# Optimization experiments

Hardware: AMD Instinct MI355X
Metric: run time of the kernel (lower is better)

Reference implementation:

```python
import jax, jax.numpy as jnp
import numpy as np

EMBED_DIM = 1024
NUM_HEADS = 16
HEAD_DIM = EMBED_DIM // NUM_HEADS


def setup_inputs() -> dict:
    key = jax.random.key(0)
    ks = jax.random.split(key, 9)
    B, T, D = 4, 2048, EMBED_DIM
    s = 1.0 / np.sqrt(D)
    inp = {
        "x": jax.random.normal(ks[0], (B, T, D), dtype=jnp.float32),
        "Wq": jax.random.normal(ks[1], (D, D), dtype=jnp.float32) * s,
        "bq": jnp.zeros((D,), dtype=jnp.float32),
        "Wk": jax.random.normal(ks[2], (D, D), dtype=jnp.float32) * s,
        "bk": jnp.zeros((D,), dtype=jnp.float32),
        "Wv": jax.random.normal(ks[3], (D, D), dtype=jnp.float32) * s,
        "bv": jnp.zeros((D,), dtype=jnp.float32),
        "Wo": jax.random.normal(ks[4], (D, D), dtype=jnp.float32) * s,
        "bo": jnp.zeros((D,), dtype=jnp.float32),
    }
    return inp


def _attn(x, Wq, bq, Wk, bk, Wv, bv, Wo, bo):
    B, T, D = x.shape
    H, Hd = NUM_HEADS, HEAD_DIM
    # projections: Linear uses y = x @ W^T + b; here W stored as (D, D) acting as W^T already
    q = (x @ Wq + bq).reshape(B, T, H, Hd).transpose(0, 2, 1, 3)  # [B,H,T,Hd]
    k = (x @ Wk + bk).reshape(B, T, H, Hd).transpose(0, 2, 1, 3)
    v = (x @ Wv + bv).reshape(B, T, H, Hd).transpose(0, 2, 1, 3)
    scores = jnp.einsum("bhqd,bhkd->bhqk", q, k) / np.sqrt(Hd)  # [B,H,T,T]
    causal = jnp.tril(jnp.ones((T, T), dtype=bool))
    scores = jnp.where(causal, scores, -jnp.inf)
    w = jax.nn.softmax(scores, axis=-1)
    out = jnp.einsum("bhqk,bhkd->bhqd", w, v)  # [B,H,T,Hd]
    out = out.transpose(0, 2, 1, 3).reshape(B, T, D)
    return out @ Wo + bo


def reference(x, Wq, bq, Wk, bk, Wv, bv, Wo, bo):
    return _attn(x, Wq, bq, Wk, bk, Wv, bv, Wo, bo)
```

## Files before the change

### kernel.cpp

```cpp
#include <hip/hip_runtime.h>
#include <cstdint>
#include <cstddef>

#define DI __device__ __forceinline__

typedef unsigned short u16;
typedef short bf16x8 __attribute__((ext_vector_type(8)));
typedef unsigned short u16x8 __attribute__((ext_vector_type(8)));
typedef float f32x4 __attribute__((ext_vector_type(4)));

static constexpr int DMODEL = 1024, T = 2048, BB = 4, NH = 16, HD = 64;
static constexpr int M = BB * T;

static constexpr size_t XB_OFF = 0;
static constexpr size_t WT_OFF = (size_t)M * DMODEL;
static constexpr size_t Q_OFF  = WT_OFF + 4ull * DMODEL * DMODEL;
static constexpr size_t K_OFF  = Q_OFF + (size_t)M * DMODEL;
static constexpr size_t V_OFF  = K_OFF + (size_t)M * DMODEL;
static constexpr size_t O_OFF  = XB_OFF;

DI u16 f2bf(float x) {
  unsigned int u = __builtin_bit_cast(unsigned int, x);
  u += 0x7fffu + ((u >> 16) & 1u);
  return (u16)(u >> 16);
}

DI unsigned int cvtpk_bf16(float a, float b) {
  unsigned int r;
  asm("v_cvt_pk_bf16_f32 %0, %1, %2" : "=v"(r) : "v"(a), "v"(b));
  return r;
}

DI void gld_lds16(const void* g, void* l) {
  __builtin_amdgcn_global_load_lds(
      (const __attribute__((address_space(1))) void*)g,
      (__attribute__((address_space(3))) void*)l, 16, 0, 0);
}

__global__ void k_cast(const float* __restrict__ in, u16* __restrict__ out) {
  size_t i = (size_t)(blockIdx.x * 256 + threadIdx.x) * 8;
  float4 a = *(const float4*)(in + i);
  float4 b = *(const float4*)(in + i + 4);
  u16x8 v;
  v[0] = f2bf(a.x); v[1] = f2bf(a.y); v[2] = f2bf(a.z); v[3] = f2bf(a.w);
  v[4] = f2bf(b.x); v[5] = f2bf(b.y); v[6] = f2bf(b.z); v[7] = f2bf(b.w);
  *(u16x8*)(out + i) = v;
}

__global__ void k_transw(const float* __restrict__ Wq, const float* __restrict__ Wk,
                         const float* __restrict__ Wv, const float* __restrict__ Wo,
                         u16* __restrict__ WtBase) {
  __shared__ u16 tile[32][33];
  const int z = blockIdx.z;
  const float* W = z == 0 ? Wq : (z == 1 ? Wk : (z == 2 ? Wv : Wo));
  u16* Wt = WtBase + (size_t)z * DMODEL * DMODEL;
  int tx = threadIdx.x, ty = threadIdx.y;
  int c = blockIdx.x * 32 + tx;
#pragma unroll
  for (int i = 0; i < 4; ++i) {
    int r = blockIdx.y * 32 + ty + i * 8;
    tile[ty + i * 8][tx] = f2bf(W[(size_t)r * DMODEL + c]);
  }
  __syncthreads();
#pragma unroll
  for (int i = 0; i < 4; ++i) {
    int rw = blockIdx.x * 32 + ty + i * 8;
    Wt[(size_t)rw * DMODEL + blockIdx.y * 32 + tx] = tile[tx][ty + i * 8];
  }
}

template <bool SWAP>
DI void gemm_loop(const u16* __restrict__ A, const u16* __restrict__ Bt,
                  u16* As, u16* Bs, f32x4 (&acc)[4][4], int brow, int bcol, int tid) {
  const int wave = tid >> 6, lane = tid & 63;
  const int g = lane >> 4, l15 = lane & 15;
  const int wr = wave >> 1, wc = wave & 1;
  const int srow = tid >> 3, schunk = tid & 7;

  for (int k0 = 0; k0 < DMODEL; k0 += 64) {
    __syncthreads();
#pragma unroll
    for (int j = 0; j < 4; ++j) {
      int r = j * 32 + srow;
      int cs = (schunk ^ (r & 7)) * 8;
      gld_lds16(A + (size_t)(brow + r) * DMODEL + k0 + cs, (char*)As + j * 4096 + wave * 1024);
      gld_lds16(Bt + (size_t)(bcol + r) * DMODEL + k0 + cs, (char*)Bs + j * 4096 + wave * 1024);
    }
    __syncthreads();
#pragma unroll
    for (int kh = 0; kh < 2; ++kh) {
      bf16x8 af[4], bfr[4];
#pragma unroll
      for (int m = 0; m < 4; ++m) {
        int r = wr * 64 + m * 16 + l15;
        int ch = (kh * 4 + g) ^ (r & 7);
        af[m] = *(const bf16x8*)((const char*)As + r * 128 + ch * 16);
      }
#pragma unroll
      for (int n = 0; n < 4; ++n) {
        int r = wc * 64 + n * 16 + l15;
        int ch = (kh * 4 + g) ^ (r & 7);
        bfr[n] = *(const bf16x8*)((const char*)Bs + r * 128 + ch * 16);
      }
#pragma unroll
      for (int m = 0; m < 4; ++m)
#pragma unroll
        for (int n = 0; n < 4; ++n) {
          if (SWAP)
            acc[m][n] = __builtin_amdgcn_mfma_f32_16x16x32_bf16(bfr[n], af[m], acc[m][n], 0, 0, 0);
          else
            acc[m][n] = __builtin_amdgcn_mfma_f32_16x16x32_bf16(af[m], bfr[n], acc[m][n], 0, 0, 0);
        }
    }
  }
}

__launch_bounds__(256, 2)
__global__ void k_gemm_qkv(const u16* __restrict__ A, const u16* __restrict__ Wt,
                           const float* __restrict__ bq, const float* __restrict__ bk,
                           const float* __restrict__ bv,
                           u16* __restrict__ Qo, u16* __restrict__ Ko,
                           u16* __restrict__ VTo) {
  __shared__ u16 As[128 * 64];
  __shared__ u16 Bs[128 * 64];
  const int z = blockIdx.z;
  const u16* Bt = Wt + (size_t)z * DMODEL * DMODEL;

  const int tid = threadIdx.x;
  const int wave = tid >> 6, lane = tid & 63;
  const int g = lane >> 4, l15 = lane & 15;
  const int brow = blockIdx.x * 128, bcol = blockIdx.y * 128;
  const int wr = wave >> 1, wc = wave & 1;

  f32x4 acc[4][4] = {};

  if (z == 2) {
    gemm_loop<true>(A, Bt, As, Bs, acc, brow, bcol, tid);
#pragma unroll
    for (int m = 0; m < 4; ++m) {
      int trow = brow + wr * 64 + m * 16 + l15;
      int b = trow >> 11, t = trow & 2047;
      int kt = t >> 6, tin = t & 63;
#pragma unroll
      for (int n = 0; n < 4; ++n)
#pragma unroll
        for (int r = 0; r < 4; ++r) {
          int dg = bcol + wc * 64 + n * 16 + g * 4 + r;
          float v = acc[m][n][r] + bv[dg];
          int h = dg >> 6, dd = dg & 63;
          VTo[(((size_t)(b * NH + h) * 32 + kt) << 12) + dd * 64 + tin] = f2bf(v);
        }
    }
  } else {
    gemm_loop<false>(A, Bt, As, Bs, acc, brow, bcol, tid);
    const float* bias = z == 0 ? bq : bk;
    u16* out = z == 0 ? Qo : Ko;
    const float scale = z == 0 ? 0.125f * 1.4426950408889634f : 1.0f;
#pragma unroll
    for (int m = 0; m < 4; ++m)
#pragma unroll
      for (int n = 0; n < 4; ++n) {
        int col = bcol + wc * 64 + n * 16 + l15;
        float bias_v = bias[col];
        int h = col >> 6, d = col & 63;
#pragma unroll
        for (int r = 0; r < 4; ++r) {
          int row = brow + wr * 64 + m * 16 + g * 4 + r;
          int b = row >> 11, t = row & 2047;
          float v = (acc[m][n][r] + bias_v) * scale;
          out[(((size_t)(b * NH + h) * T + t) << 6) + d] = f2bf(v);
        }
      }
  }
}

__launch_bounds__(256, 2)
__global__ void k_gemm_out(const u16* __restrict__ A, const u16* __restrict__ Bt,
                           const float* __restrict__ bias, float* __restrict__ out) {
  __shared__ u16 As[128 * 64];
  __shared__ u16 Bs[128 * 64];
  const int tid = threadIdx.x;
  const int wave = tid >> 6, lane = tid & 63;
  const int g = lane >> 4, l15 = lane & 15;
  const int brow = blockIdx.x * 128, bcol = blockIdx.y * 128;
  const int wr = wave >> 1, wc = wave & 1;

  f32x4 acc[4][4] = {};
  gemm_loop<false>(A, Bt, As, Bs, acc, brow, bcol, tid);

#pragma unroll
  for (int m = 0; m < 4; ++m)
#pragma unroll
    for (int n = 0; n < 4; ++n) {
      int col = bcol + wc * 64 + n * 16 + l15;
      float bias_v = bias[col];
#pragma unroll
      for (int r = 0; r < 4; ++r) {
        int row = brow + wr * 64 + m * 16 + g * 4 + r;
        out[(size_t)row * DMODEL + col] = acc[m][n][r] + bias_v;
      }
    }
}

__launch_bounds__(256, 4)
__global__ void k_attn(const u16* __restrict__ Qw, const u16* __restrict__ Kw,
                       const u16* __restrict__ VTw, u16* __restrict__ Ow) {
  __shared__ u16 Ks[2][64 * 64];
  __shared__ u16 Vt[2][64 * 64];
  __shared__ u16 Ot[64 * 64];

  const int tid = threadIdx.x;
  const int wave = tid >> 6, lane = tid & 63;
  const int g = lane >> 4, l15 = lane & 15;
  const int tl = (l15 & 3) | ((l15 & 4) << 1) | ((l15 & 8) >> 1);
  const int l = blockIdx.x;
  const int xcd = l & 7, w = l >> 3;
  const int bh = xcd + ((w & 7) << 3);
  const int qp = w >> 3;
  const u16* Qb = Qw + (size_t)bh * T * HD;
  const u16* Kb = Kw + (size_t)bh * T * HD;
  const u16* Vb = VTw + (size_t)bh * HD * T;
  const int b = bh >> 4, h = bh & 15;
  const int krow = tid >> 3, kchunk = tid & 7;

  for (int half = 0; half < 2; ++half) {
    const int qt = half == 0 ? (31 - qp) : qp;
    const int ntiles = qt + 1;

    bf16x8 qf[2];
    {
      int qrow = qt * 64 + wave * 16 + l15;
#pragma unroll
      for (int kh = 0; kh < 2; ++kh)
        qf[kh] = *(const bf16x8*)(Qb + (size_t)qrow * HD + kh * 32 + g * 8);
    }

    f32x4 oacc[4] = {};
    float lrun = 0.f;

#pragma unroll
    for (int j = 0; j < 2; ++j) {
      int r = j * 32 + krow;
      gld_lds16(Kb + (size_t)r * HD + (kchunk ^ (r & 7)) * 8,
                (char*)(Ks[0]) + j * 4096 + wave * 1024);
      gld_lds16(Vb + r * 64 + (kchunk ^ (r & 7)) * 8,
                (char*)(Vt[0]) + j * 4096 + wave * 1024);
    }

    for (int kt = 0; kt < ntiles; ++kt) {
      __syncthreads();
      const int cur = kt & 1;
      const bool havenext = (kt + 1 < ntiles);

      if (havenext) {
#pragma unroll
        for (int j = 0; j < 2; ++j) {
          int r = j * 32 + krow;
          gld_lds16(Kb + (size_t)((kt + 1) * 64 + r) * HD + (kchunk ^ (r & 7)) * 8,
                    (char*)(Ks[cur ^ 1]) + j * 4096 + wave * 1024);
          gld_lds16(Vb + ((size_t)(kt + 1) << 12) + r * 64 + (kchunk ^ (r & 7)) * 8,
                    (char*)(Vt[cur ^ 1]) + j * 4096 + wave * 1024);
        }
      }

      bf16x8 kf[2][4];
#pragma unroll
      for (int kh = 0; kh < 2; ++kh)
#pragma unroll
        for (int n = 0; n < 4; ++n) {
          int rr = n * 16 + tl;
          int ch = (kh * 4 + g) ^ (rr & 7);
          kf[kh][n] = *(const bf16x8*)((const char*)(Ks[cur]) + rr * 128 + ch * 16);
        }

      f32x4 s[4] = {};
      __builtin_amdgcn_s_setprio(1);
#pragma unroll
      for (int kh = 0; kh < 2; ++kh)
#pragma unroll
        for (int n = 0; n < 4; ++n)
          s[n] = __builtin_amdgcn_mfma_f32_16x16x32_bf16(kf[kh][n], qf[kh], s[n], 0, 0, 0);
      __builtin_amdgcn_s_setprio(0);

      if (kt == qt) {
        int q_in = wave * 16 + l15;
#pragma unroll
        for (int n = 0; n < 4; ++n)
#pragma unroll
          for (int r = 0; r < 4; ++r) {
            int kv_in = n * 16 + (g & 1) * 8 + (g >> 1) * 4 + r;
            if (kv_in > q_in) s[n][r] = -1e30f;
          }
      }

      float ps0 = 0.f, ps1 = 0.f, ps2 = 0.f, ps3 = 0.f;
#pragma unroll
      for (int n = 0; n < 4; ++n) {
        float p0 = exp2f(s[n][0]);
        float p1 = exp2f(s[n][1]);
        float p2 = exp2f(s[n][2]);
        float p3 = exp2f(s[n][3]);
        s[n][0] = p0; s[n][1] = p1; s[n][2] = p2; s[n][3] = p3;
        ps0 += p0; ps1 += p1; ps2 += p2; ps3 += p3;
      }
      lrun += (ps0 + ps1) + (ps2 + ps3);

      __builtin_amdgcn_s_setprio(1);
#pragma unroll
      for (int kvh = 0; kvh < 2; ++kvh) {
        const int nlo = kvh * 2, nhi = kvh * 2 + 1;
        unsigned int L0 = cvtpk_bf16(s[nlo][0], s[nlo][1]);
        unsigned int L1 = cvtpk_bf16(s[nlo][2], s[nlo][3]);
        unsigned int H0 = cvtpk_bf16(s[nhi][0], s[nhi][1]);
        unsigned int H1 = cvtpk_bf16(s[nhi][2], s[nhi][3]);
        asm volatile("v_permlane32_swap_b32 %0, %1" : "+v"(L0), "+v"(H0));
        asm volatile("v_permlane32_swap_b32 %0, %1" : "+v"(L1), "+v"(H1));
        bf16x8 pb;
        unsigned int* pw = (unsigned int*)&pb;
        pw[0] = L0; pw[1] = L1; pw[2] = H0; pw[3] = H1;

        const int ch = ((kvh * 4 + g) ^ (l15 & 7)) * 16;
#pragma unroll
        for (int n = 0; n < 4; ++n) {
          bf16x8 an = *(const bf16x8*)((const char*)(Vt[cur]) + (n * 16 + l15) * 128 + ch);
          oacc[n] = __builtin_amdgcn_mfma_f32_16x16x32_bf16(an, pb, oacc[n], 0, 0, 0);
        }
      }
      __builtin_amdgcn_s_setprio(0);
    }

    {
      float ltot = lrun;
      ltot += __shfl_xor(ltot, 16);
      ltot += __shfl_xor(ltot, 32);
      float inv = 1.f / ltot;
      char* otb = (char*)Ot;
#pragma unroll
      for (int n = 0; n < 4; ++n)
#pragma unroll
        for (int i = 0; i < 2; ++i) {
          unsigned int w2 = cvtpk_bf16(oacc[n][2 * i] * inv, oacc[n][2 * i + 1] * inv);
          int didx = n * 8 + g * 2 + i;
          int off = (wave * 16 + l15) * 128 + ((didx * 4) ^ ((l15 & 7) << 4));
          *(unsigned int*)(otb + off) = w2;
        }
      __syncthreads();
      int q = tid >> 2, seg = tid & 3;
      uint4 c0 = *(const uint4*)(otb + q * 128 + (((seg * 2) ^ (q & 7)) << 4));
      uint4 c1 = *(const uint4*)(otb + q * 128 + (((seg * 2 + 1) ^ (q & 7)) << 4));
      u16* dst = Ow + ((size_t)b * T + qt * 64 + q) * DMODEL + h * 64 + seg * 16;
      *(uint4*)dst = c0;
      *(uint4*)(dst + 8) = c1;
    }
  }
}

extern "C" void kernel_launch(void* const* d_in, const int* in_sizes, int n_in,
                              void* d_out, int out_size, void* d_ws, size_t ws_size,
                              hipStream_t stream) {
  const float* x  = (const float*)d_in[0];
  const float* Wq = (const float*)d_in[1];
  const float* bq = (const float*)d_in[2];
  const float* Wk = (const float*)d_in[3];
  const float* bk = (const float*)d_in[4];
  const float* Wv = (const float*)d_in[5];
  const float* bv = (const float*)d_in[6];
  const float* Wo = (const float*)d_in[7];
  const float* bo = (const float*)d_in[8];
  float* out = (float*)d_out;
  u16* ws = (u16*)d_ws;

  k_cast<<<4096, 256, 0, stream>>>(x, ws + XB_OFF);
  k_transw<<<dim3(32, 32, 4), dim3(32, 8), 0, stream>>>(Wq, Wk, Wv, Wo, ws + WT_OFF);
  k_gemm_qkv<<<dim3(64, 8, 3), 256, 0, stream>>>(ws + XB_OFF, ws + WT_OFF, bq, bk, bv,
                                                 ws + Q_OFF, ws + K_OFF, ws + V_OFF);
  k_attn<<<1024, 256, 0, stream>>>(ws + Q_OFF, ws + K_OFF, ws + V_OFF, ws + O_OFF);
  k_gemm_out<<<dim3(64, 8), 256, 0, stream>>>(ws + O_OFF, ws + WT_OFF + 3ull * DMODEL * DMODEL,
                                              bo, out);
}
```

Before: 155.1 us.

## Use two waves per attention block, each processing 32 query rows

```diff
diff --git a/kernel.cpp b/kernel.cpp
--- a/kernel.cpp
+++ b/kernel.cpp
@@ -202,7 +202,7 @@
     }
 }
 
-__launch_bounds__(256, 4)
+__launch_bounds__(128, 2)
 __global__ void k_attn(const u16* __restrict__ Qw, const u16* __restrict__ Kw,
                        const u16* __restrict__ VTw, u16* __restrict__ Ow) {
   __shared__ u16 Ks[2][64 * 64];
@@ -221,30 +221,31 @@
   const u16* Kb = Kw + (size_t)bh * T * HD;
   const u16* Vb = VTw + (size_t)bh * HD * T;
   const int b = bh >> 4, h = bh & 15;
-  const int krow = tid >> 3, kchunk = tid & 7;
+  const int srow8 = lane >> 3, schunk = lane & 7;
 
   for (int half = 0; half < 2; ++half) {
     const int qt = half == 0 ? (31 - qp) : qp;
     const int ntiles = qt + 1;
 
-    bf16x8 qf[2];
-    {
-      int qrow = qt * 64 + wave * 16 + l15;
+    bf16x8 qf[2][2];
+#pragma unroll
+    for (int set = 0; set < 2; ++set) {
+      int qrow = qt * 64 + wave * 32 + set * 16 + l15;
 #pragma unroll
       for (int kh = 0; kh < 2; ++kh)
-        qf[kh] = *(const bf16x8*)(Qb + (size_t)qrow * HD + kh * 32 + g * 8);
-    }
-
-    f32x4 oacc[4] = {};
-    float lrun = 0.f;
-
-#pragma unroll
-    for (int j = 0; j < 2; ++j) {
-      int r = j * 32 + krow;
-      gld_lds16(Kb + (size_t)r * HD + (kchunk ^ (r & 7)) * 8,
-                (char*)(Ks[0]) + j * 4096 + wave * 1024);
-      gld_lds16(Vb + r * 64 + (kchunk ^ (r & 7)) * 8,
-                (char*)(Vt[0]) + j * 4096 + wave * 1024);
+        qf[set][kh] = *(const bf16x8*)(Qb + (size_t)qrow * HD + kh * 32 + g * 8);
+    }
+
+    f32x4 oacc[2][4] = {};
+    float lrun0 = 0.f, lrun1 = 0.f;
+
+#pragma unroll
+    for (int j = 0; j < 4; ++j) {
+      int r = j * 16 + wave * 8 + srow8;
+      gld_lds16(Kb + (size_t)r * HD + (schunk ^ (r & 7)) * 8,
+                (char*)(Ks[0]) + j * 2048 + wave * 1024);
+      gld_lds16(Vb + r * 64 + (schunk ^ (r & 7)) * 8,
+                (char*)(Vt[0]) + j * 2048 + wave * 1024);
     }
 
     for (int kt = 0; kt < ntiles; ++kt) {
@@ -254,12 +255,12 @@
 
       if (havenext) {
 #pragma unroll
-        for (int j = 0; j < 2; ++j) {
-          int r = j * 32 + krow;
-          gld_lds16(Kb + (size_t)((kt + 1) * 64 + r) * HD + (kchunk ^ (r & 7)) * 8,
-                    (char*)(Ks[cur ^ 1]) + j * 4096 + wave * 1024);
-          gld_lds16(Vb + ((size_t)(kt + 1) << 12) + r * 64 + (kchunk ^ (r & 7)) * 8,
-                    (char*)(Vt[cur ^ 1]) + j * 4096 + wave * 1024);
+        for (int j = 0; j < 4; ++j) {
+          int r = j * 16 + wave * 8 + srow8;
+          gld_lds16(Kb + (size_t)((kt + 1) * 64 + r) * HD + (schunk ^ (r & 7)) * 8,
+                    (char*)(Ks[cur ^ 1]) + j * 2048 + wave * 1024);
+          gld_lds16(Vb + ((size_t)(kt + 1) << 12) + r * 64 + (schunk ^ (r & 7)) * 8,
+                    (char*)(Vt[cur ^ 1]) + j * 2048 + wave * 1024);
         }
       }
 
@@ -273,84 +274,127 @@
           kf[kh][n] = *(const bf16x8*)((const char*)(Ks[cur]) + rr * 128 + ch * 16);
         }
 
-      f32x4 s[4] = {};
+      f32x4 s[2][4] = {};
       __builtin_amdgcn_s_setprio(1);
 #pragma unroll
       for (int kh = 0; kh < 2; ++kh)
 #pragma unroll
-        for (int n = 0; n < 4; ++n)
-          s[n] = __builtin_amdgcn_mfma_f32_16x16x32_bf16(kf[kh][n], qf[kh], s[n], 0, 0, 0);
+        for (int n = 0; n < 4; ++n) {
+          s[0][n] = __builtin_amdgcn_mfma_f32_16x16x32_bf16(kf[kh][n], qf[0][kh], s[0][n], 0, 0, 0);
+          s[1][n] = __builtin_amdgcn_mfma_f32_16x16x32_bf16(kf[kh][n], qf[1][kh], s[1][n], 0, 0, 0);
+        }
       __builtin_amdgcn_s_setprio(0);
 
       if (kt == qt) {
-        int q_in = wave * 16 + l15;
-#pragma unroll
-        for (int n = 0; n < 4; ++n)
-#pragma unroll
-          for (int r = 0; r < 4; ++r) {
-            int kv_in = n * 16 + (g & 1) * 8 + (g >> 1) * 4 + r;
-            if (kv_in > q_in) s[n][r] = -1e30f;
-          }
-      }
-
-      float ps0 = 0.f, ps1 = 0.f, ps2 = 0.f, ps3 = 0.f;
-#pragma unroll
-      for (int n = 0; n < 4; ++n) {
-        float p0 = exp2f(s[n][0]);
-        float p1 = exp2f(s[n][1]);
-        float p2 = exp2f(s[n][2]);
-        float p3 = exp2f(s[n][3]);
-        s[n][0] = p0; s[n][1] = p1; s[n][2] = p2; s[n][3] = p3;
-        ps0 += p0; ps1 += p1; ps2 += p2; ps3 += p3;
-      }
-      lrun += (ps0 + ps1) + (ps2 + ps3);
+#pragma unroll
+        for (int set = 0; set < 2; ++set) {
+          int q_in = wave * 32 + set * 16 + l15;
+#pragma unroll
+          for (int n = 0; n < 4; ++n)
+#pragma unroll
+            for (int r = 0; r < 4; ++r) {
+              int kv_in = n * 16 + (g & 1) * 8 + (g >> 1) * 4 + r;
+              if (kv_in > q_in) s[set][n][r] = -1e30f;
+            }
+        }
+      }
+
+      {
+        float ps0 = 0.f, ps1 = 0.f, ps2 = 0.f, ps3 = 0.f;
+#pragma unroll
+        for (int n = 0; n < 4; ++n) {
+          float p0 = exp2f(s[0][n][0]);
+          float p1 = exp2f(s[0][n][1]);
+          float p2 = exp2f(s[0][n][2]);
+          float p3 = exp2f(s[0][n][3]);
+          s[0][n][0] = p0; s[0][n][1] = p1; s[0][n][2] = p2; s[0][n][3] = p3;
+          ps0 += p0; ps1 += p1; ps2 += p2; ps3 += p3;
+        }
+        lrun0 += (ps0 + ps1) + (ps2 + ps3);
+      }
+      {
+        float ps0 = 0.f, ps1 = 0.f, ps2 = 0.f, ps3 = 0.f;
+#pragma unroll
+        for (int n = 0; n < 4; ++n) {
+          float p0 = exp2f(s[1][n][0]);
+          float p1 = exp2f(s[1][n][1]);
+          float p2 = exp2f(s[1][n][2]);
+          float p3 = exp2f(s[1][n][3]);
+          s[1][n][0] = p0; s[1][n][1] = p1; s[1][n][2] = p2; s[1][n][3] = p3;
+          ps0 += p0; ps1 += p1; ps2 += p2; ps3 += p3;
+        }
+        lrun1 += (ps0 + ps1) + (ps2 + ps3);
+      }
 
       __builtin_amdgcn_s_setprio(1);
 #pragma unroll
       for (int kvh = 0; kvh < 2; ++kvh) {
         const int nlo = kvh * 2, nhi = kvh * 2 + 1;
-        unsigned int L0 = cvtpk_bf16(s[nlo][0], s[nlo][1]);
-        unsigned int L1 = cvtpk_bf16(s[nlo][2], s[nlo][3]);
-        unsigned int H0 = cvtpk_bf16(s[nhi][0], s[nhi][1]);
-        unsigned int H1 = cvtpk_bf16(s[nhi][2], s[nhi][3]);
-        asm volatile("v_permlane32_swap_b32 %0, %1" : "+v"(L0), "+v"(H0));
-        asm volatile("v_permlane32_swap_b32 %0, %1" : "+v"(L1), "+v"(H1));
-        bf16x8 pb;
-        unsigned int* pw = (unsigned int*)&pb;
-        pw[0] = L0; pw[1] = L1; pw[2] = H0; pw[3] = H1;
+        unsigned int A0 = cvtpk_bf16(s[0][nlo][0], s[0][nlo][1]);
+        unsigned int A1 = cvtpk_bf16(s[0][nlo][2], s[0][nlo][3]);
+        unsigned int B0 = cvtpk_bf16(s[0][nhi][0], s[0][nhi][1]);
+        unsigned int B1 = cvtpk_bf16(s[0][nhi][2], s[0][nhi][3]);
+        asm volatile("v_permlane32_swap_b32 %0, %1" : "+v"(A0), "+v"(B0));
+        asm volatile("v_permlane32_swap_b32 %0, %1" : "+v"(A1), "+v"(B1));
+        bf16x8 pb0;
+        {
+          unsigned int* pw = (unsigned int*)&pb0;
+          pw[0] = A0; pw[1] = A1; pw[2] = B0; pw[3] = B1;
+        }
+        unsigned int C0 = cvtpk_bf16(s[1][nlo][0], s[1][nlo][1]);
+        unsigned int C1 = cvtpk_bf16(s[1][nlo][2], s[1][nlo][3]);
+        unsigned int D0 = cvtpk_bf16(s[1][nhi][0], s[1][nhi][1]);
+        unsigned int D1 = cvtpk_bf16(s[1][nhi][2], s[1][nhi][3]);
+        asm volatile("v_permlane32_swap_b32 %0, %1" : "+v"(C0), "+v"(D0));
+        asm volatile("v_permlane32_swap_b32 %0, %1" : "+v"(C1), "+v"(D1));
+        bf16x8 pb1;
+        {
+          unsigned int* pw = (unsigned int*)&pb1;
+          pw[0] = C0; pw[1] = C1; pw[2] = D0; pw[3] = D1;
+        }
 
         const int ch = ((kvh * 4 + g) ^ (l15 & 7)) * 16;
 #pragma unroll
         for (int n = 0; n < 4; ++n) {
           bf16x8 an = *(const bf16x8*)((const char*)(Vt[cur]) + (n * 16 + l15) * 128 + ch);
-          oacc[n] = __builtin_amdgcn_mfma_f32_16x16x32_bf16(an, pb, oacc[n], 0, 0, 0);
+          oacc[0][n] = __builtin_amdgcn_mfma_f32_16x16x32_bf16(an, pb0, oacc[0][n], 0, 0, 0);
+          oacc[1][n] = __builtin_amdgcn_mfma_f32_16x16x32_bf16(an, pb1, oacc[1][n], 0, 0, 0);
         }
       }
       __builtin_amdgcn_s_setprio(0);
     }
 
     {
-      float ltot = lrun;
-      ltot += __shfl_xor(ltot, 16);
-      ltot += __shfl_xor(ltot, 32);
-      float inv = 1.f / ltot;
+      float lt0 = lrun0;
+      lt0 += __shfl_xor(lt0, 16);
+      lt0 += __shfl_xor(lt0, 32);
+      float lt1 = lrun1;
+      lt1 += __shfl_xor(lt1, 16);
+      lt1 += __shfl_xor(lt1, 32);
+      float inv0 = 1.f / lt0, inv1 = 1.f / lt1;
       char* otb = (char*)Ot;
 #pragma unroll
       for (int n = 0; n < 4; ++n)
 #pragma unroll
         for (int i = 0; i < 2; ++i) {
-          unsigned int w2 = cvtpk_bf16(oacc[n][2 * i] * inv, oacc[n][2 * i + 1] * inv);
           int didx = n * 8 + g * 2 + i;
-          int off = (wave * 16 + l15) * 128 + ((didx * 4) ^ ((l15 & 7) << 4));
-          *(unsigned int*)(otb + off) = w2;
+          int cswz = (didx * 4) ^ ((l15 & 7) << 4);
+          unsigned int w0 = cvtpk_bf16(oacc[0][n][2 * i] * inv0, oacc[0][n][2 * i + 1] * inv0);
+          *(unsigned int*)(otb + (wave * 32 + l15) * 128 + cswz) = w0;
+          unsigned int w1 = cvtpk_bf16(oacc[1][n][2 * i] * inv1, oacc[1][n][2 * i + 1] * inv1);
+          *(unsigned int*)(otb + (wave * 32 + 16 + l15) * 128 + cswz) = w1;
         }
       __syncthreads();
-      int q = tid >> 2, seg = tid & 3;
-      uint4 c0 = *(const uint4*)(otb + q * 128 + (((seg * 2) ^ (q & 7)) << 4));
-      uint4 c1 = *(const uint4*)(otb + q * 128 + (((seg * 2 + 1) ^ (q & 7)) << 4));
-      u16* dst = Ow + ((size_t)b * T + qt * 64 + q) * DMODEL + h * 64 + seg * 16;
-      *(uint4*)dst = c0;
-      *(uint4*)(dst + 8) = c1;
+#pragma unroll
+      for (int i = 0; i < 2; ++i) {
+        int q = i * 32 + (tid >> 2), seg = tid & 3;
+        uint4 c0 = *(const uint4*)(otb + q * 128 + (((seg * 2) ^ (q & 7)) << 4));
+        uint4 c1 = *(const uint4*)(otb + q * 128 + (((seg * 2 + 1) ^ (q & 7)) << 4));
+        u16* dst = Ow + ((size_t)b * T + qt * 64 + q) * DMODEL + h * 64 + seg * 16;
+        *(uint4*)dst = c0;
+        *(uint4*)(dst + 8) = c1;
+      }
+      __syncthreads();
     }
   }
 }
@@ -374,7 +418,7 @@
   k_transw<<<dim3(32, 32, 4), dim3(32, 8), 0, stream>>>(Wq, Wk, Wv, Wo, ws + WT_OFF);
   k_gemm_qkv<<<dim3(64, 8, 3), 256, 0, stream>>>(ws + XB_OFF, ws + WT_OFF, bq, bk, bv,
                                                  ws + Q_OFF, ws + K_OFF, ws + V_OFF);
-  k_attn<<<1024, 256, 0, stream>>>(ws + Q_OFF, ws + K_OFF, ws + V_OFF, ws + O_OFF);
+  k_attn<<<1024, 128, 0, stream>>>(ws + Q_OFF, ws + K_OFF, ws + V_OFF, ws + O_OFF);
   k_gemm_out<<<dim3(64, 8), 256, 0, stream>>>(ws + O_OFF, ws + WT_OFF + 3ull * DMODEL * DMODEL,
                                               bo, out);
 }
```

Measured after the change: 157.4 us. No clear change (+1.5%).
